# Kernel tuning notes

Measured on AMD Instinct MI355X. Metric: run time of the kernel, lower is better.

## Reference

```python
import jax, jax.numpy as jnp
import numpy as np

D = 768
B = 32
N = 768


def setup_inputs() -> dict:
    key = jax.random.key(0)
    k1, k2, k3, k4 = jax.random.split(key, 4)
    stdv = 1.0 / np.sqrt(D)
    X = jax.random.normal(k1, (B, N, D), dtype=jnp.float32)
    adj = jax.random.uniform(k2, (B, N, N), dtype=jnp.float32)
    W_l = jax.random.uniform(k3, (D, D), dtype=jnp.float32, minval=-stdv, maxval=stdv)
    W_l1 = jax.random.uniform(k4, (D, D), dtype=jnp.float32, minval=-stdv, maxval=stdv)
    return {"X": X, "adj": adj, "W_l": W_l, "W_l1": W_l1}


def _row_normalize(adj):
    # rowsum^-1 with inf -> 0 (rows summing to zero stay zero)
    rowsum = adj.sum(axis=-1, keepdims=True)  # [B, N, 1]
    r_inv = jnp.where(rowsum == 0, 0.0, 1.0 / rowsum)
    return adj * r_inv


def reference(X, adj, W_l, W_l1):
    # X: [B, N, D], adj: [B, N, N]
    adj_n = _row_normalize(adj)
    e1 = jnp.einsum('bnd,de->bne', X, W_l1)        # message transform
    e11 = jnp.einsum('bnm,bmd->bnd', adj_n, e1)    # aggregate
    X1 = jnp.einsum('bnd,de->bne', X, W_l)         # self transform
    h = X1 + e11
    return jax.nn.leaky_relu(h, negative_slope=0.01)
```

## Files before the change

kernel.cpp:

```cpp
#include <hip/hip_runtime.h>
#include <hip/hip_bf16.h>
#include <cstdint>
#include <cstddef>

#define BN_ROWS 24576
#define DD 768
#define BE (768*768)
#define BM 192
#define BN_T 192
#define BK 32
#define ABUF 12288
#define BUFSZ 24576

typedef __attribute__((ext_vector_type(8))) short bf16x8;
typedef __attribute__((ext_vector_type(4))) float f32x4;

static __device__ __forceinline__ unsigned short f2bf(float f) {
  unsigned int u = __builtin_bit_cast(unsigned int, f);
  unsigned int lsb = (u >> 16) & 1u;
  u += 0x7fffu + lsb;
  return (unsigned short)(u >> 16);
}


#define PREP_CX 4096
#define PREP_WT 144
#define PREP_AN 6144

__global__ __launch_bounds__(256) void prep(const float* __restrict__ X,
                                            const float* __restrict__ adj,
                                            const float* __restrict__ Wl,
                                            const float* __restrict__ Wl1,
                                            unsigned short* __restrict__ Xb,
                                            unsigned short* __restrict__ adjnb,
                                            unsigned short* __restrict__ WlT,
                                            unsigned short* __restrict__ Wl1T) {
  __shared__ float tile[64][65];
  const int bid = blockIdx.x;

  if (bid < PREP_CX) {
    const int n4 = (BN_ROWS * DD) / 4;
    for (int i = bid * 256 + threadIdx.x; i < n4; i += PREP_CX * 256) {
      float4 v = reinterpret_cast<const float4*>(X)[i];
      ushort4 o;
      o.x = f2bf(v.x); o.y = f2bf(v.y); o.z = f2bf(v.z); o.w = f2bf(v.w);
      reinterpret_cast<ushort4*>(Xb)[i] = o;
    }
  } else if (bid < PREP_CX + PREP_WT) {
    const int tb = bid - PREP_CX;
    const int tr = tb / 12, tc = tb % 12;
    const int c = threadIdx.x & 63, r0 = threadIdx.x >> 6;
    const float* srcs[2] = {Wl, Wl1};
    unsigned short* dsts[2] = {WlT, Wl1T};
    #pragma unroll
    for (int m = 0; m < 2; ++m) {
      const float* src = srcs[m];
      #pragma unroll
      for (int i = 0; i < 16; ++i) {
        int r = r0 + i * 4;
        tile[r][c] = src[(size_t)(tr * 64 + r) * DD + tc * 64 + c];
      }
      __syncthreads();
      unsigned short* dst = dsts[m];
      #pragma unroll
      for (int i = 0; i < 16; ++i) {
        int r2 = r0 + i * 4;
        dst[(size_t)(tc * 64 + r2) * DD + tr * 64 + c] = f2bf(tile[c][r2]);
      }
      __syncthreads();
    }
  } else {
    const int rb = bid - (PREP_CX + PREP_WT);
    const int wid = threadIdx.x >> 6, lane = threadIdx.x & 63;
    const int row = rb * 4 + wid;
    const float4* a = reinterpret_cast<const float4*>(adj + (size_t)row * DD);
    float4 v[3];
    float s = 0.f;
    #pragma unroll
    for (int i = 0; i < 3; ++i) {
      v[i] = a[i * 64 + lane];
      s += (v[i].x + v[i].y) + (v[i].z + v[i].w);
    }
    #pragma unroll
    for (int off = 32; off; off >>= 1) s += __shfl_down(s, off);
    s = __shfl(s, 0);
    float rinv = (s == 0.f) ? 0.f : 1.f / s;
    ushort4* o = reinterpret_cast<ushort4*>(adjnb + (size_t)row * DD);
    #pragma unroll
    for (int i = 0; i < 3; ++i) {
      ushort4 u;
      u.x = f2bf(v[i].x * rinv); u.y = f2bf(v[i].y * rinv);
      u.z = f2bf(v[i].z * rinv); u.w = f2bf(v[i].w * rinv);
      o[i * 64 + lane] = u;
    }
  }
}


template<int MODE>
__global__ __launch_bounds__(256, 2) void gemm4(
    const unsigned short* __restrict__ P0,
    const unsigned short* __restrict__ P1,
    const unsigned short* __restrict__ P2,
    const unsigned short* __restrict__ P3,
    void* __restrict__ outp)
{
  __shared__ char smem[2 * BUFSZ];
  constexpr int NT = MODE ? 48 : 24;
  const int tid = threadIdx.x, lane = tid & 63;
  const int wid = tid >> 6;
  const int wr = wid >> 1, wc = wid & 1;

  const int logical = (blockIdx.x & 7) * 64 + (blockIdx.x >> 3);

  const unsigned short *Ab0, *Bb0, *Ab1 = nullptr, *Bb1 = nullptr;
  int mt, nt, b;
  if (MODE == 0) {
    mt = logical >> 2; nt = logical & 3;
    b = mt >> 2;
    Ab0 = P0 + (size_t)mt * BM * DD;
    Bb0 = P1 + (size_t)nt * BN_T * DD;
  } else {
    b = logical >> 4; int r = logical & 15; mt = r >> 2; nt = r & 3;
    size_t bo = (size_t)b * BE;
    Ab0 = P0 + bo + (size_t)mt * BM * DD;
    Bb0 = P1 + bo + (size_t)nt * BN_T * DD;
    Ab1 = P2 + bo + (size_t)mt * BM * DD;
    Bb1 = P3 + (size_t)nt * BN_T * DD;
  }

  const int r_in = lane >> 2;
  const int s_in = lane & 3;

  auto stage = [&](int s) {
    const int buf = (s & 1) * BUFSZ;
    const unsigned short *Ab, *Bb;
    int kk;
    if (MODE == 1 && s >= 24) { kk = s - 24; Ab = Ab1; Bb = Bb1; }
    else                      { kk = s;      Ab = Ab0; Bb = Bb0; }
    #pragma unroll
    for (int i = 0; i < 6; ++i) {
      int chunk = wid * 6 + i;
      bool isA = chunk < 12;
      int c = isA ? chunk : chunk - 12;
      int row = c * 16 + r_in;
      int slot = s_in ^ ((row >> 1) & 3);
      const unsigned short* src = (isA ? Ab : Bb) + (size_t)row * DD + kk * BK + slot * 8;
      __builtin_amdgcn_global_load_lds(
          (const __attribute__((address_space(1))) void*)src,
          (__attribute__((address_space(3))) void*)(smem + buf + (isA ? 0 : ABUF) + c * 1024),
          16, 0, 0);
    }
  };

  const int ks = lane >> 4;
  auto frag = [&](int off, int row) -> bf16x8 {
    int slot = ks ^ ((row >> 1) & 3);
    return *reinterpret_cast<const bf16x8*>(smem + off + row * 64 + slot * 16);
  };

  f32x4 acc[6][6] = {};
  const int arow = wr * 96 + (lane & 15);
  const int brow = wc * 96 + (lane & 15);

  stage(0);

  for (int t = 0; t < NT; ++t) {
    asm volatile("s_waitcnt vmcnt(0)" ::: "memory");
    __builtin_amdgcn_s_barrier();

    if (t + 1 < NT) stage(t + 1);

    const int bufA = (t & 1) * BUFSZ;
    const int bufB = bufA + ABUF;
    bf16x8 a[6], bg[6];
    #pragma unroll
    for (int i = 0; i < 6; ++i) a[i] = frag(bufA, arow + i * 16);
    #pragma unroll
    for (int i = 0; i < 6; ++i) bg[i] = frag(bufB, brow + i * 16);

    __builtin_amdgcn_s_setprio(1);
    #pragma unroll
    for (int ni = 0; ni < 6; ++ni)
      #pragma unroll
      for (int mi = 0; mi < 6; ++mi)
        acc[mi][ni] = __builtin_amdgcn_mfma_f32_16x16x32_bf16(a[mi], bg[ni], acc[mi][ni], 0, 0, 0);
    __builtin_amdgcn_s_setprio(0);
  }

  if (MODE == 0) {
    unsigned short* ob = (unsigned short*)outp + (size_t)b * BE;
    const int mloc = (mt & 3) * BM + wr * 96 + (lane >> 4) * 4;
    #pragma unroll
    for (int mi = 0; mi < 6; ++mi)
      #pragma unroll
      for (int ni = 0; ni < 6; ++ni) {
        int m = mloc + mi * 16;
        int d = nt * BN_T + wc * 96 + ni * 16 + (lane & 15);
        f32x4 v = acc[mi][ni];
        ushort4 o;
        o.x = f2bf(v[0]); o.y = f2bf(v[1]); o.z = f2bf(v[2]); o.w = f2bf(v[3]);
        *reinterpret_cast<ushort4*>(ob + (size_t)d * DD + m) = o;
      }
  } else {
    float* ob = (float*)outp + (size_t)b * BE;
    const int mloc = mt * BM + wr * 96 + (lane >> 4) * 4;
    #pragma unroll
    for (int mi = 0; mi < 6; ++mi)
      #pragma unroll
      for (int ni = 0; ni < 6; ++ni) {
        int m = mloc + mi * 16;
        int n = nt * BN_T + wc * 96 + ni * 16 + (lane & 15);
        f32x4 v = acc[mi][ni];
        #pragma unroll
        for (int j = 0; j < 4; ++j) {
          float x = v[j];
          ob[(size_t)(m + j) * DD + n] = x > 0.f ? x : 0.01f * x;
        }
      }
  }
}


extern "C" void kernel_launch(void* const* d_in, const int* in_sizes, int n_in,
                              void* d_out, int out_size, void* d_ws, size_t ws_size,
                              hipStream_t stream) {
  const float* X   = (const float*)d_in[0];
  const float* adj = (const float*)d_in[1];
  const float* Wl  = (const float*)d_in[2];
  const float* Wl1 = (const float*)d_in[3];
  float* out = (float*)d_out;

  char* ws = (char*)d_ws;
  const size_t SZ = (size_t)BN_ROWS * DD * 2;
  unsigned short* Xb    = (unsigned short*)(ws);
  unsigned short* adjnb = (unsigned short*)(ws + SZ);
  unsigned short* e1T   = (unsigned short*)(ws + 2 * SZ);
  unsigned short* WlT   = (unsigned short*)(ws + 3 * SZ);
  unsigned short* Wl1T  = (unsigned short*)(ws + 3 * SZ + (size_t)BE * 2);

  prep<<<PREP_CX + PREP_WT + PREP_AN, 256, 0, stream>>>(X, adj, Wl, Wl1,
                                                        Xb, adjnb, WlT, Wl1T);
  gemm4<0><<<512, 256, 0, stream>>>(Xb, Wl1T, nullptr, nullptr, e1T);
  gemm4<1><<<512, 256, 0, stream>>>(adjnb, e1T, Xb, WlT, out);
}
```

Before: 146.6 us.

## Store B operands in MFMA fragment layout and load them directly to registers

```diff
diff --git a/kernel.cpp b/kernel.cpp
--- a/kernel.cpp
+++ b/kernel.cpp
@@ -14,6 +14,7 @@
 
 typedef __attribute__((ext_vector_type(8))) short bf16x8;
 typedef __attribute__((ext_vector_type(4))) float f32x4;
+typedef __attribute__((ext_vector_type(8))) unsigned short u16x8;
 
 static __device__ __forceinline__ unsigned short f2bf(float f) {
   unsigned int u = __builtin_bit_cast(unsigned int, f);
@@ -23,8 +24,10 @@
 }
 
 
+
 #define PREP_CX 4096
 #define PREP_WT 144
+#define PREP_FL 288
 #define PREP_AN 6144
 
 __global__ __launch_bounds__(256) void prep(const float* __restrict__ X,
@@ -50,27 +53,32 @@
     const int tb = bid - PREP_CX;
     const int tr = tb / 12, tc = tb % 12;
     const int c = threadIdx.x & 63, r0 = threadIdx.x >> 6;
-    const float* srcs[2] = {Wl, Wl1};
-    unsigned short* dsts[2] = {WlT, Wl1T};
-    #pragma unroll
-    for (int m = 0; m < 2; ++m) {
-      const float* src = srcs[m];
-      #pragma unroll
-      for (int i = 0; i < 16; ++i) {
-        int r = r0 + i * 4;
-        tile[r][c] = src[(size_t)(tr * 64 + r) * DD + tc * 64 + c];
-      }
-      __syncthreads();
-      unsigned short* dst = dsts[m];
-      #pragma unroll
-      for (int i = 0; i < 16; ++i) {
-        int r2 = r0 + i * 4;
-        dst[(size_t)(tc * 64 + r2) * DD + tr * 64 + c] = f2bf(tile[c][r2]);
-      }
-      __syncthreads();
-    }
+    #pragma unroll
+    for (int i = 0; i < 16; ++i) {
+      int r = r0 + i * 4;
+      tile[r][c] = Wl1[(size_t)(tr * 64 + r) * DD + tc * 64 + c];
+    }
+    __syncthreads();
+    #pragma unroll
+    for (int i = 0; i < 16; ++i) {
+      int r2 = r0 + i * 4;
+      Wl1T[(size_t)(tc * 64 + r2) * DD + tr * 64 + c] = f2bf(tile[c][r2]);
+    }
+  } else if (bid < PREP_CX + PREP_WT + PREP_FL) {
+    const int b2 = bid - (PREP_CX + PREP_WT);
+    const int wg = b2 * 4 + (threadIdx.x >> 6);
+    const int lane = threadIdx.x & 63;
+    const int d0 = (wg % 96) * 8;
+    const int e = (wg / 96) * 64 + lane;
+    u16x8 o;
+    #pragma unroll
+    for (int j = 0; j < 8; ++j)
+      o[j] = f2bf(Wl[(size_t)(d0 + j) * DD + e]);
+    const int base = ((e >> 4) * 24 + (d0 >> 5)) * 512
+                   + ((e & 15) + (((d0 >> 3) & 3) << 4)) * 8;
+    *reinterpret_cast<u16x8*>(WlT + base) = o;
   } else {
-    const int rb = bid - (PREP_CX + PREP_WT);
+    const int rb = bid - (PREP_CX + PREP_WT + PREP_FL);
     const int wid = threadIdx.x >> 6, lane = threadIdx.x & 63;
     const int row = rb * 4 + wid;
     const float4* a = reinterpret_cast<const float4*>(adj + (size_t)row * DD);
@@ -96,48 +104,28 @@
   }
 }
 
-
-template<int MODE>
-__global__ __launch_bounds__(256, 2) void gemm4(
-    const unsigned short* __restrict__ P0,
-    const unsigned short* __restrict__ P1,
-    const unsigned short* __restrict__ P2,
-    const unsigned short* __restrict__ P3,
-    void* __restrict__ outp)
+__global__ __launch_bounds__(256, 2) void gemm_e1(
+    const unsigned short* __restrict__ Xb,
+    const unsigned short* __restrict__ W1T,
+    unsigned short* __restrict__ e1T)
 {
   __shared__ char smem[2 * BUFSZ];
-  constexpr int NT = MODE ? 48 : 24;
+  constexpr int NT = 24;
   const int tid = threadIdx.x, lane = tid & 63;
   const int wid = tid >> 6;
   const int wr = wid >> 1, wc = wid & 1;
 
   const int logical = (blockIdx.x & 7) * 64 + (blockIdx.x >> 3);
-
-  const unsigned short *Ab0, *Bb0, *Ab1 = nullptr, *Bb1 = nullptr;
-  int mt, nt, b;
-  if (MODE == 0) {
-    mt = logical >> 2; nt = logical & 3;
-    b = mt >> 2;
-    Ab0 = P0 + (size_t)mt * BM * DD;
-    Bb0 = P1 + (size_t)nt * BN_T * DD;
-  } else {
-    b = logical >> 4; int r = logical & 15; mt = r >> 2; nt = r & 3;
-    size_t bo = (size_t)b * BE;
-    Ab0 = P0 + bo + (size_t)mt * BM * DD;
-    Bb0 = P1 + bo + (size_t)nt * BN_T * DD;
-    Ab1 = P2 + bo + (size_t)mt * BM * DD;
-    Bb1 = P3 + (size_t)nt * BN_T * DD;
-  }
+  const int mt = logical >> 2, nt = logical & 3;
+  const int b = mt >> 2;
+  const unsigned short* Ab0 = Xb + (size_t)mt * BM * DD;
+  const unsigned short* Bb0 = W1T + (size_t)nt * BN_T * DD;
 
   const int r_in = lane >> 2;
   const int s_in = lane & 3;
 
   auto stage = [&](int s) {
     const int buf = (s & 1) * BUFSZ;
-    const unsigned short *Ab, *Bb;
-    int kk;
-    if (MODE == 1 && s >= 24) { kk = s - 24; Ab = Ab1; Bb = Bb1; }
-    else                      { kk = s;      Ab = Ab0; Bb = Bb0; }
     #pragma unroll
     for (int i = 0; i < 6; ++i) {
       int chunk = wid * 6 + i;
@@ -145,7 +133,7 @@
       int c = isA ? chunk : chunk - 12;
       int row = c * 16 + r_in;
       int slot = s_in ^ ((row >> 1) & 3);
-      const unsigned short* src = (isA ? Ab : Bb) + (size_t)row * DD + kk * BK + slot * 8;
+      const unsigned short* src = (isA ? Ab0 : Bb0) + (size_t)row * DD + s * BK + slot * 8;
       __builtin_amdgcn_global_load_lds(
           (const __attribute__((address_space(1))) void*)src,
           (__attribute__((address_space(3))) void*)(smem + buf + (isA ? 0 : ABUF) + c * 1024),
@@ -164,13 +152,10 @@
   const int brow = wc * 96 + (lane & 15);
 
   stage(0);
-
   for (int t = 0; t < NT; ++t) {
     asm volatile("s_waitcnt vmcnt(0)" ::: "memory");
     __builtin_amdgcn_s_barrier();
-
     if (t + 1 < NT) stage(t + 1);
-
     const int bufA = (t & 1) * BUFSZ;
     const int bufB = bufA + ABUF;
     bf16x8 a[6], bg[6];
@@ -178,7 +163,6 @@
     for (int i = 0; i < 6; ++i) a[i] = frag(bufA, arow + i * 16);
     #pragma unroll
     for (int i = 0; i < 6; ++i) bg[i] = frag(bufB, brow + i * 16);
-
     __builtin_amdgcn_s_setprio(1);
     #pragma unroll
     for (int ni = 0; ni < 6; ++ni)
@@ -188,37 +172,135 @@
     __builtin_amdgcn_s_setprio(0);
   }
 
-  if (MODE == 0) {
-    unsigned short* ob = (unsigned short*)outp + (size_t)b * BE;
-    const int mloc = (mt & 3) * BM + wr * 96 + (lane >> 4) * 4;
-    #pragma unroll
-    for (int mi = 0; mi < 6; ++mi)
+  unsigned short* ob = e1T + (size_t)b * BE;
+  const int m0 = (mt & 3) * BM + wr * 96 + (lane >> 4) * 4;
+  const int l15 = lane & 15;
+  #pragma unroll
+  for (int mi = 0; mi < 6; ++mi)
+    #pragma unroll
+    for (int ni = 0; ni < 6; ++ni) {
+      int m = m0 + mi * 16;
+      int cb = nt * 12 + wc * 6 + ni;
+      int fa = (cb * 24 + (m >> 5)) * 512
+             + (l15 + (((m >> 3) & 3) << 4)) * 8 + (m & 7);
+      f32x4 v = acc[mi][ni];
+      ushort4 o;
+      o.x = f2bf(v[0]); o.y = f2bf(v[1]); o.z = f2bf(v[2]); o.w = f2bf(v[3]);
+      *reinterpret_cast<ushort4*>(ob + fa) = o;
+    }
+}
+
+__global__ __launch_bounds__(256, 2) void gemm_bg(
+    const unsigned short* __restrict__ adjnb,
+    const unsigned short* __restrict__ e1T,
+    const unsigned short* __restrict__ Xb,
+    const unsigned short* __restrict__ WlT,
+    float* __restrict__ out)
+{
+  __shared__ char smem[24576];
+  constexpr int NT = 48;
+  const int tid = threadIdx.x, lane = tid & 63;
+  const int wid = tid >> 6;
+  const int wr = wid >> 1, wc = wid & 1;
+
+  const int logical = (blockIdx.x & 7) * 64 + (blockIdx.x >> 3);
+  const int b = logical >> 4;
+  const int r = logical & 15;
+  const int mt = r >> 2, nt = r & 3;
+  const size_t bo = (size_t)b * BE;
+  const unsigned short* A0 = adjnb + bo + (size_t)mt * BM * DD;
+  const unsigned short* A1 = Xb + bo + (size_t)mt * BM * DD;
+  const unsigned short* B0 = e1T + bo;
+  const unsigned short* B1 = WlT;
+
+  const int r_in = lane >> 2;
+  const int s_in = lane & 3;
+  const int colblk0 = nt * 12 + wc * 6;
+
+  auto stage = [&](int s) {
+    int sc = s < NT ? s : 0;
+    const unsigned short* base = (sc >= 24) ? A1 : A0;
+    int kk = (sc >= 24) ? sc - 24 : sc;
+    const int buf = (s & 1) * 12288;
+    #pragma unroll
+    for (int i = 0; i < 3; ++i) {
+      int chunk = wid * 3 + i;
+      int row = chunk * 16 + r_in;
+      int slot = s_in ^ ((row >> 1) & 3);
+      const unsigned short* src = base + (size_t)row * DD + kk * BK + slot * 8;
+      __builtin_amdgcn_global_load_lds(
+          (const __attribute__((address_space(1))) void*)src,
+          (__attribute__((address_space(3))) void*)(smem + buf + chunk * 1024),
+          16, 0, 0);
+    }
+  };
+
+  auto loadB = [&](int s, bf16x8* dst) {
+    int sc = s < NT ? s : 0;
+    const unsigned short* base = (sc >= 24) ? B1 : B0;
+    int kk = (sc >= 24) ? sc - 24 : sc;
+    #pragma unroll
+    for (int ni = 0; ni < 6; ++ni)
+      dst[ni] = *reinterpret_cast<const bf16x8*>(
+          base + ((colblk0 + ni) * 24 + kk) * 512 + lane * 8);
+  };
+
+  const int ks = lane >> 4;
+  auto rdA = [&](int off, int row) -> bf16x8 {
+    int slot = ks ^ ((row >> 1) & 3);
+    return *reinterpret_cast<const bf16x8*>(smem + off + row * 64 + slot * 16);
+  };
+
+  f32x4 acc[6][6] = {};
+  const int arow = wr * 96 + (lane & 15);
+  bf16x8 bA[6], bB[6];
+
+  auto body = [&](int bufo, bf16x8* bfr) {
+    #pragma unroll
+    for (int mh = 0; mh < 2; ++mh) {
+      bf16x8 a[3];
       #pragma unroll
-      for (int ni = 0; ni < 6; ++ni) {
-        int m = mloc + mi * 16;
-        int d = nt * BN_T + wc * 96 + ni * 16 + (lane & 15);
-        f32x4 v = acc[mi][ni];
-        ushort4 o;
-        o.x = f2bf(v[0]); o.y = f2bf(v[1]); o.z = f2bf(v[2]); o.w = f2bf(v[3]);
-        *reinterpret_cast<ushort4*>(ob + (size_t)d * DD + m) = o;
+      for (int i = 0; i < 3; ++i) a[i] = rdA(bufo, arow + mh * 48 + i * 16);
+      __builtin_amdgcn_s_setprio(1);
+      #pragma unroll
+      for (int mi = 0; mi < 3; ++mi)
+        #pragma unroll
+        for (int ni = 0; ni < 6; ++ni)
+          acc[mh * 3 + mi][ni] = __builtin_amdgcn_mfma_f32_16x16x32_bf16(
+              a[mi], bfr[ni], acc[mh * 3 + mi][ni], 0, 0, 0);
+      __builtin_amdgcn_s_setprio(0);
+    }
+  };
+
+  stage(0); loadB(0, bA);
+  for (int t = 0; t < NT; t += 2) {
+    asm volatile("s_waitcnt vmcnt(6)" ::: "memory");
+    __builtin_amdgcn_s_barrier();
+    stage(t + 1); loadB(t + 1, bB);
+    body(0, bA);
+    asm volatile("s_waitcnt vmcnt(6)" ::: "memory");
+    __builtin_amdgcn_s_barrier();
+    stage(t + 2); loadB(t + 2, bA);
+    body(12288, bB);
+  }
+  asm volatile("s_waitcnt vmcnt(0)" ::: "memory");
+
+  float* ob = out + bo;
+  const int m0 = mt * BM + wr * 96 + (lane >> 4) * 4;
+  const int l15 = lane & 15;
+  #pragma unroll
+  for (int mi = 0; mi < 6; ++mi)
+    #pragma unroll
+    for (int ni = 0; ni < 6; ++ni) {
+      int m = m0 + mi * 16;
+      int n = nt * BN_T + wc * 96 + ni * 16 + l15;
+      f32x4 v = acc[mi][ni];
+      #pragma unroll
+      for (int j = 0; j < 4; ++j) {
+        float x = v[j];
+        ob[(size_t)(m + j) * DD + n] = x > 0.f ? x : 0.01f * x;
       }
-  } else {
-    float* ob = (float*)outp + (size_t)b * BE;
-    const int mloc = mt * BM + wr * 96 + (lane >> 4) * 4;
-    #pragma unroll
-    for (int mi = 0; mi < 6; ++mi)
-      #pragma unroll
-      for (int ni = 0; ni < 6; ++ni) {
-        int m = mloc + mi * 16;
-        int n = nt * BN_T + wc * 96 + ni * 16 + (lane & 15);
-        f32x4 v = acc[mi][ni];
-        #pragma unroll
-        for (int j = 0; j < 4; ++j) {
-          float x = v[j];
-          ob[(size_t)(m + j) * DD + n] = x > 0.f ? x : 0.01f * x;
-        }
-      }
-  }
+    }
 }
 
 
@@ -239,8 +321,8 @@
   unsigned short* WlT   = (unsigned short*)(ws + 3 * SZ);
   unsigned short* Wl1T  = (unsigned short*)(ws + 3 * SZ + (size_t)BE * 2);
 
-  prep<<<PREP_CX + PREP_WT + PREP_AN, 256, 0, stream>>>(X, adj, Wl, Wl1,
-                                                        Xb, adjnb, WlT, Wl1T);
-  gemm4<0><<<512, 256, 0, stream>>>(Xb, Wl1T, nullptr, nullptr, e1T);
-  gemm4<1><<<512, 256, 0, stream>>>(adjnb, e1T, Xb, WlT, out);
-}
+  prep<<<PREP_CX + PREP_WT + PREP_FL + PREP_AN, 256, 0, stream>>>(
+      X, adj, Wl, Wl1, Xb, adjnb, WlT, Wl1T);
+  gemm_e1<<<512, 256, 0, stream>>>(Xb, Wl1T, e1T);
+  gemm_bg<<<512, 256, 0, stream>>>(adjnb, e1T, Xb, WlT, out);
+}
```

Result: faster. 139.0 us (-5.2%).
